# Optimization experiments

Hardware: AMD Instinct MI355X
Metric: run time of the kernel (lower is better)

Reference implementation:

```python
import jax, jax.numpy as jnp
import numpy as np

BS = 512
N_BOXES = 30   # num_boxes*3 in the torch module
K = 15
HID = 128
EMB = 64
FEAT = HID + EMB + 2  # 194


def _knn_idx(x, k):
    # x: (bs, n, 4); per-sample kNN (self excluded), matching pyg knn_graph with batch
    d = jnp.sum((x[:, :, None, :] - x[:, None, :, :]) ** 2, axis=-1)  # (bs, n, n)
    n = x.shape[1]
    d = d + jnp.eye(n, dtype=x.dtype) * 1e9  # exclude self-loops
    _, idx = jax.lax.top_k(-d, k)  # k nearest sources j for each target i
    return idx  # (bs, n, k)


def _edge_conv(x, idx, Wa, ba, Wb, bb):
    # EdgeConv: out_i = max_j mlp([x_i, x_j - x_i]), aggr='max'
    xj = jax.vmap(lambda xb, ib: xb[ib])(x, idx)            # (bs, n, k, F)
    xi = jnp.broadcast_to(x[:, :, None, :], xj.shape)        # (bs, n, k, F)
    m = jnp.concatenate([xi, xj - xi], axis=-1)              # (bs, n, k, 2F)
    h = jax.nn.relu(jnp.einsum('bnkf,hf->bnkh', m, Wa) + ba)
    h = jnp.einsum('bnkh,oh->bnko', h, Wb) + bb
    return jnp.max(h, axis=2)                                # (bs, n, HID)


def _q(nodes, emb, Wi, bi, Wma, bma, Wmb, bmb, Wca, bca, Wcb, bcb):
    bs, n, _ = nodes.shape
    idx = _knn_idx(nodes, K)
    cats = jnp.repeat(jnp.arange(3), n // 3)                 # [0]*10+[1]*10+[2]*10
    cls = jax.nn.relu(emb[cats])                             # (n, EMB)
    cls = jnp.broadcast_to(cls[None], (bs, n, EMB))
    tar = jnp.zeros((bs, n, 2), nodes.dtype)                 # tanh(zeros) = 0
    init = jnp.concatenate([jax.nn.relu(nodes @ Wi.T + bi), cls, tar], axis=-1)
    h = jax.nn.relu(_edge_conv(init, idx, Wma, bma, Wmb, bmb))
    h = jax.nn.relu(h @ Wca.T + bca)
    out = h @ Wcb.T + bcb                                    # (bs, n, 1)
    return out.reshape(bs, -1)


def setup_inputs() -> dict:
    key = jax.random.key(0)
    ks = jax.random.split(key, 22)
    rn = lambda k, shp: (jax.random.normal(k, shp) * 0.05).astype(jnp.float32)
    return {
        'state': jax.random.normal(ks[0], (BS, N_BOXES * 2), jnp.float32),
        'action': jax.random.normal(ks[1], (BS, N_BOXES * 2), jnp.float32),
        'W_init1': rn(ks[2], (HID, 4)), 'b_init1': rn(ks[3], (HID,)),
        'emb1': rn(ks[4], (3, EMB)),
        'W_m1a': rn(ks[5], (HID, 2 * FEAT)), 'b_m1a': rn(ks[6], (HID,)),
        'W_m1b': rn(ks[7], (HID, HID)), 'b_m1b': rn(ks[8], (HID,)),
        'W_c1a': rn(ks[9], (HID, HID)), 'b_c1a': rn(ks[10], (HID,)),
        'W_c1b': rn(ks[11], (1, HID)), 'b_c1b': rn(ks[12], (1,)),
        'W_init2': rn(ks[13], (HID, 4)), 'b_init2': rn(ks[14], (HID,)),
        'emb2': rn(ks[15], (3, EMB)),
        'W_c2a': rn(ks[16], (HID, HID)), 'b_c2a': rn(ks[17], (HID,)),
        'W_c2b': rn(ks[18], (1, HID)), 'b_c2b': rn(ks[19], (1,)),
    }


def reference(state, action, W_init1, b_init1, emb1, W_m1a, b_m1a, W_m1b, b_m1b,
              W_c1a, b_c1a, W_c1b, b_c1b, W_init2, b_init2, emb2,
              W_c2a, b_c2a, W_c2b, b_c2b):
    bs = state.shape[0]
    # Q1 node layout: interleaved per-box [sx, sy, ax, ay]
    nodes1 = jnp.concatenate([state.reshape(bs, N_BOXES, 2),
                              action.reshape(bs, N_BOXES, 2)], axis=-1)
    q1 = _q(nodes1, emb1, W_init1, b_init1, W_m1a, b_m1a, W_m1b, b_m1b,
            W_c1a, b_c1a, W_c1b, b_c1b)
    # Q2 node layout (faithful to torch bug): cat along dim 1 then view(-1, 4)
    nodes2 = jnp.concatenate([state, action], axis=1).reshape(bs, N_BOXES, 4)
    # conv1_2 reuses mlp1_1 weights (faithful to torch source)
    q2 = _q(nodes2, emb2, W_init2, b_init2, W_m1a, b_m1a, W_m1b, b_m1b,
            W_c2a, b_c2a, W_c2b, b_c2b)
    return (q1, q2)
```

## Files before the change

### kernel.cpp

```cpp
#include <hip/hip_runtime.h>

#define BSZ 512
#define NNODE 30
#define KNBR 15
#define HID 128
#define MTOT (BSZ*NNODE)

typedef __attribute__((ext_vector_type(8))) __bf16 bf16x8;
typedef __attribute__((ext_vector_type(4))) float f32x4;

__device__ __forceinline__ float frelu(float x){ return x > 0.f ? x : 0.f; }

__device__ __forceinline__ void node_coords(const float* __restrict__ st,
                                            const float* __restrict__ ac,
                                            int b, int n, int qsel, float c[4]) {
    if (qsel == 0) {
        c[0] = st[b*60 + 2*n];     c[1] = st[b*60 + 2*n + 1];
        c[2] = ac[b*60 + 2*n];     c[3] = ac[b*60 + 2*n + 1];
    } else {
        int base = 4*n;
        if (base < 60) {
            c[0]=st[b*60+base]; c[1]=st[b*60+base+1]; c[2]=st[b*60+base+2]; c[3]=st[b*60+base+3];
        } else {
            int a = base - 60;
            c[0]=ac[b*60+a]; c[1]=ac[b*60+a+1]; c[2]=ac[b*60+a+2]; c[3]=ac[b*60+a+3];
        }
    }
}

__global__ void k_prep(const float* __restrict__ Wa,  const float* __restrict__ Wb,
                       const float* __restrict__ Wca1,const float* __restrict__ Wca2,
                       const float* __restrict__ ba,
                       const float* __restrict__ emb1,const float* __restrict__ emb2,
                       __bf16* __restrict__ Wc16, __bf16* __restrict__ Wb16,
                       __bf16* __restrict__ Wca16_1, __bf16* __restrict__ Wca16_2,
                       float* __restrict__ cls1A, float* __restrict__ cls1B,
                       float* __restrict__ cls2A, float* __restrict__ cls2B) {
    int blk = blockIdx.x;
    if (blk < 320) {
        int t = blk*256 + threadIdx.x;
        if (t < 32768) {
            int o = t >> 7, h = t & 127;
            float v = (o < 128) ? (Wa[o*388 + h] - Wa[o*388 + 194 + h])
                                : Wa[(o-128)*388 + 194 + h];
            Wc16[t] = (__bf16)v;
        } else if (t < 49152) { int u = t - 32768; Wb16[u]    = (__bf16)Wb[u]; }
        else if (t < 65536)   { int u = t - 49152; Wca16_1[u] = (__bf16)Wca1[u]; }
        else                  { int u = t - 65536; Wca16_2[u] = (__bf16)Wca2[u]; }
    } else {
        int o = threadIdx.x;
        if (o >= 128) return;
        const float* emb = (blk == 320) ? emb1  : emb2;
        float* cA        = (blk == 320) ? cls1A : cls2A;
        float* cB        = (blk == 320) ? cls1B : cls2B;
        for (int c = 0; c < 3; ++c) {
            float sA = ba[o], sB = 0.f;
            for (int e = 0; e < 64; ++e) {
                float r  = frelu(emb[c*64 + e]);
                float wl = Wa[o*388 + 128 + e];
                float wr = Wa[o*388 + 194 + 128 + e];
                sA += (wl - wr) * r;
                sB += wr * r;
            }
            cA[c*128 + o] = sA;
            cB[c*128 + o] = sB;
        }
    }
}

__global__ void __launch_bounds__(256, 4) k_fused(
        const float* __restrict__ st, const float* __restrict__ ac,
        const float* __restrict__ Wi1, const float* __restrict__ bi1,
        const float* __restrict__ Wi2, const float* __restrict__ bi2,
        const __bf16* __restrict__ Wc16,
        const float* __restrict__ cls1A, const float* __restrict__ cls1B,
        const float* __restrict__ cls2A, const float* __restrict__ cls2B,
        const __bf16* __restrict__ Wb16, const float* __restrict__ bb,
        const __bf16* __restrict__ Wca16_1, const float* __restrict__ bca1,
        const float* __restrict__ Wcb1, const float* __restrict__ bcb1,
        const __bf16* __restrict__ Wca16_2, const float* __restrict__ bca2,
        const float* __restrict__ Wcb2, const float* __restrict__ bcb2,
        float* __restrict__ out) {
    __shared__ __align__(16) union UVE {
        __bf16 Vf[2][4][4][16][8];
        __bf16 El[32*136];
    } uVE;
    __shared__ __align__(16) __bf16 Al[30*136];
    __shared__ __align__(16) __bf16 Bl[30*136];
    __shared__ int idxs[30*16];
    __shared__ __align__(16) union UCR {
        float coords[30][4];
        float redh[4][16];
    } uCR;

    int tid  = threadIdx.x;
    int lane = tid & 63, wid = tid >> 6;
    int l15  = lane & 15, g = (lane >> 4) & 3;
    int bid  = blockIdx.x;
    int q    = bid >> 9, b = bid & 511;

    const float* Wi   = q ? Wi2 : Wi1;
    const float* bi   = q ? bi2 : bi1;
    const float* clsA = q ? cls2A : cls1A;
    const float* clsB = q ? cls2B : cls1B;
    const __bf16* Wca16 = q ? Wca16_2 : Wca16_1;
    const float* bca  = q ? bca2 : bca1;
    const float* Wcb  = q ? Wcb2 : Wcb1;
    const float* bcb  = q ? bcb2 : bcb1;

    if (tid < 30) {
        float c[4]; node_coords(st, ac, b, tid, q, c);
        uCR.coords[tid][0]=c[0]; uCR.coords[tid][1]=c[1];
        uCR.coords[tid][2]=c[2]; uCR.coords[tid][3]=c[3];
    }
    __syncthreads();

    if (tid < 30) {
        int i = tid;
        float ci0=uCR.coords[i][0], ci1=uCR.coords[i][1], ci2=uCR.coords[i][2], ci3=uCR.coords[i][3];
        float d[30];
        #pragma unroll
        for (int j = 0; j < 30; ++j) {
            float d0 = ci0-uCR.coords[j][0], d1 = ci1-uCR.coords[j][1];
            float d2 = ci2-uCR.coords[j][2], d3 = ci3-uCR.coords[j][3];
            d[j] = d0*d0 + d1*d1 + d2*d2 + d3*d3;
        }
        unsigned mask = 1u << i;
        for (int k = 0; k < KNBR; ++k) {
            float best = 3.4e38f; int bj = 0;
            #pragma unroll
            for (int j = 0; j < 30; ++j) {
                bool ok = !((mask >> j) & 1u) && (d[j] < best);
                if (ok) { best = d[j]; bj = j; }
            }
            mask |= 1u << bj;
            idxs[i*16 + k] = bj;
        }
        idxs[i*16 + 15] = idxs[i*16];
    } else if (tid >= 32) {
        for (int it = tid - 32; it < 512; it += 224) {
            int row = it & 15, g2 = (it >> 4) & 3, kk2 = (it >> 6) & 3, mt2 = it >> 8;
            int m = mt2*16 + row;
            bf16x8 v8;
            if (m < 30) {
                float c0=uCR.coords[m][0], c1=uCR.coords[m][1],
                      c2=uCR.coords[m][2], c3=uCR.coords[m][3];
                #pragma unroll
                for (int e = 0; e < 8; ++e) {
                    int h = kk2*32 + g2*8 + e;
                    v8[e] = (__bf16)frelu(bi[h] + Wi[h*4+0]*c0 + Wi[h*4+1]*c1
                                                + Wi[h*4+2]*c2 + Wi[h*4+3]*c3);
                }
            } else {
                #pragma unroll
                for (int e = 0; e < 8; ++e) v8[e] = (__bf16)0.f;
            }
            *(bf16x8*)&uVE.Vf[mt2][kk2][g2][row][0] = v8;
        }
    }
    __syncthreads();

    {
        int mt = wid & 1, half = wid >> 1;
        bf16x8 af[4];
        #pragma unroll
        for (int kk = 0; kk < 4; ++kk) af[kk] = *(const bf16x8*)&uVE.Vf[mt][kk][g][l15][0];
        f32x4 acc[8];
        #pragma unroll
        for (int nc = 0; nc < 8; ++nc) acc[nc] = (f32x4){0.f,0.f,0.f,0.f};
        #pragma unroll
        for (int nc = 0; nc < 8; ++nc) {
            int o256 = half*128 + nc*16 + l15;
            bf16x8 wf[4];
            #pragma unroll
            for (int kk = 0; kk < 4; ++kk)
                wf[kk] = *(const bf16x8*)(Wc16 + o256*128 + kk*32 + g*8);
            #pragma unroll
            for (int kk = 0; kk < 4; ++kk)
                acc[nc] = __builtin_amdgcn_mfma_f32_16x16x32_bf16(af[kk], wf[kk], acc[nc], 0, 0, 0);
        }
        const float* cls = half ? clsB : clsA;
        __bf16* dst = half ? Bl : Al;
        #pragma unroll
        for (int nc = 0; nc < 8; ++nc) {
            #pragma unroll
            for (int r = 0; r < 4; ++r) {
                int m = mt*16 + g*4 + r;
                if (m < 30) {
                    int o = nc*16 + l15;
                    int cat = m / 10;
                    dst[m*136 + o] = (__bf16)(acc[nc][r] + cls[cat*128 + o]);
                }
            }
        }
    }
    __syncthreads();

    {
        for (int ch = 0; ch < 2; ++ch) {
            bf16x8 wbf[4][4];
            #pragma unroll
            for (int oc = 0; oc < 4; ++oc)
                #pragma unroll
                for (int kk = 0; kk < 4; ++kk)
                    wbf[oc][kk] = *(const bf16x8*)(Wb16 + ((ch*4+oc)*16 + l15)*128 + kk*32 + g*8);
            float bbv[4];
            #pragma unroll
            for (int oc = 0; oc < 4; ++oc) bbv[oc] = bb[(ch*4+oc)*16 + l15];

            for (int i = wid; i < 30; i += 4) {
                int nb = idxs[i*16 + l15];
                bf16x8 hf[4];
                #pragma unroll
                for (int kk = 0; kk < 4; ++kk) {
                    bf16x8 pa = *(const bf16x8*)&Al[i*136  + kk*32 + g*8];
                    bf16x8 pb = *(const bf16x8*)&Bl[nb*136 + kk*32 + g*8];
                    bf16x8 h;
                    #pragma unroll
                    for (int e = 0; e < 8; ++e)
                        h[e] = (__bf16)frelu((float)pa[e] + (float)pb[e]);
                    hf[kk] = h;
                }
                f32x4 acc[4];
                #pragma unroll
                for (int oc = 0; oc < 4; ++oc) acc[oc] = (f32x4){0.f,0.f,0.f,0.f};
                #pragma unroll
                for (int kk = 0; kk < 4; ++kk)
                    #pragma unroll
                    for (int oc = 0; oc < 4; ++oc)
                        acc[oc] = __builtin_amdgcn_mfma_f32_16x16x32_bf16(hf[kk], wbf[oc][kk], acc[oc], 0, 0, 0);
                #pragma unroll
                for (int oc = 0; oc < 4; ++oc) {
                    float v = fmaxf(fmaxf(acc[oc][0], acc[oc][1]), fmaxf(acc[oc][2], acc[oc][3]));
                    v = fmaxf(v, __shfl_xor(v, 16));
                    v = fmaxf(v, __shfl_xor(v, 32));
                    if (g == 0) uVE.El[i*136 + (ch*4+oc)*16 + l15] = (__bf16)frelu(v + bbv[oc]);
                }
            }
        }
        if (tid < 136) ((unsigned*)uVE.El)[2040 + tid] = 0u;
    }
    __syncthreads();

    {
        int mt = wid & 1, half = wid >> 1;
        bf16x8 ef[4];
        #pragma unroll
        for (int kk = 0; kk < 4; ++kk)
            ef[kk] = *(const bf16x8*)&uVE.El[(mt*16 + l15)*136 + kk*32 + g*8];
        float s[4] = {0.f, 0.f, 0.f, 0.f};
        #pragma unroll
        for (int nc = 0; nc < 4; ++nc) {
            int o = half*64 + nc*16 + l15;
            bf16x8 wf[4];
            #pragma unroll
            for (int kk = 0; kk < 4; ++kk)
                wf[kk] = *(const bf16x8*)(Wca16 + o*128 + kk*32 + g*8);
            f32x4 a = (f32x4){0.f,0.f,0.f,0.f};
            #pragma unroll
            for (int kk = 0; kk < 4; ++kk)
                a = __builtin_amdgcn_mfma_f32_16x16x32_bf16(ef[kk], wf[kk], a, 0, 0, 0);
            float bcav = bca[o], wcbv = Wcb[o];
            #pragma unroll
            for (int r = 0; r < 4; ++r) s[r] += frelu(a[r] + bcav) * wcbv;
        }
        #pragma unroll
        for (int r = 0; r < 4; ++r) {
            s[r] += __shfl_xor(s[r], 1);
            s[r] += __shfl_xor(s[r], 2);
            s[r] += __shfl_xor(s[r], 4);
            s[r] += __shfl_xor(s[r], 8);
        }
        if (l15 == 0) {
            #pragma unroll
            for (int r = 0; r < 4; ++r) uCR.redh[wid][g*4 + r] = s[r];
        }
    }
    __syncthreads();
    if (tid < 30) {
        int mt = tid >> 4, mr = tid & 15;
        out[q*MTOT + b*30 + tid] = uCR.redh[mt][mr] + uCR.redh[mt+2][mr] + bcb[0];
    }
}

extern "C" void kernel_launch(void* const* d_in, const int* in_sizes, int n_in,
                              void* d_out, int out_size, void* d_ws, size_t ws_size,
                              hipStream_t stream) {
    const float* state  = (const float*)d_in[0];
    const float* action = (const float*)d_in[1];
    const float* W_init1= (const float*)d_in[2];
    const float* b_init1= (const float*)d_in[3];
    const float* emb1   = (const float*)d_in[4];
    const float* W_m1a  = (const float*)d_in[5];
    const float* b_m1a  = (const float*)d_in[6];
    const float* W_m1b  = (const float*)d_in[7];
    const float* b_m1b  = (const float*)d_in[8];
    const float* W_c1a  = (const float*)d_in[9];
    const float* b_c1a  = (const float*)d_in[10];
    const float* W_c1b  = (const float*)d_in[11];
    const float* b_c1b  = (const float*)d_in[12];
    const float* W_init2= (const float*)d_in[13];
    const float* b_init2= (const float*)d_in[14];
    const float* emb2   = (const float*)d_in[15];
    const float* W_c2a  = (const float*)d_in[16];
    const float* b_c2a  = (const float*)d_in[17];
    const float* W_c2b  = (const float*)d_in[18];
    const float* b_c2b  = (const float*)d_in[19];

    __bf16* Wc16    = (__bf16*)d_ws;
    __bf16* Wb16    = Wc16 + 32768;
    __bf16* Wca16_1 = Wb16 + 16384;
    __bf16* Wca16_2 = Wca16_1 + 16384;
    float*  cls1A   = (float*)(Wca16_2 + 16384);
    float*  cls1B   = cls1A + 384;
    float*  cls2A   = cls1B + 384;
    float*  cls2B   = cls2A + 384;
    float*  out     = (float*)d_out;

    k_prep<<<322, 256, 0, stream>>>(W_m1a, W_m1b, W_c1a, W_c2a, b_m1a, emb1, emb2,
                                    Wc16, Wb16, Wca16_1, Wca16_2,
                                    cls1A, cls1B, cls2A, cls2B);

    k_fused<<<2*BSZ, 256, 0, stream>>>(state, action,
                                       W_init1, b_init1, W_init2, b_init2,
                                       Wc16, cls1A, cls1B, cls2A, cls2B,
                                       Wb16, b_m1b,
                                       Wca16_1, b_c1a, W_c1b, b_c1b,
                                       Wca16_2, b_c2a, W_c2b, b_c2b,
                                       out);
}
```

Before: 172.7 us.

## Parallelize kNN via rank counting and split EdgeConv work across warps by output half

Replaces the serial per-thread kNN selection sort (30 threads doing 15 passes) with a block-wide pairwise distance table in shared memory and a rank-counting pass, so all 256 threads take part. The distance table shares a union with the Al buffer. The EdgeConv stage is also restructured so each warp owns half of the output channels and loads that half's weights once, instead of looping over two chunks and reloading weights. Tie-breaking by index keeps the neighbour ordering deterministic. The Al and Bl buffers grow to 32 rows, and the padding rows are now written unconditionally.

```diff
diff --git a/kernel.cpp b/kernel.cpp
--- a/kernel.cpp
+++ b/kernel.cpp
@@ -85,8 +85,11 @@
         __bf16 Vf[2][4][4][16][8];
         __bf16 El[32*136];
     } uVE;
-    __shared__ __align__(16) __bf16 Al[30*136];
-    __shared__ __align__(16) __bf16 Bl[30*136];
+    __shared__ __align__(16) union UDA {
+        float  dist[30*33];
+        __bf16 Al[32*136];
+    } uDA;
+    __shared__ __align__(16) __bf16 Bl[32*136];
     __shared__ int idxs[30*16];
     __shared__ __align__(16) union UCR {
         float coords[30][4];
@@ -115,51 +118,52 @@
     }
     __syncthreads();
 
-    if (tid < 30) {
-        int i = tid;
-        float ci0=uCR.coords[i][0], ci1=uCR.coords[i][1], ci2=uCR.coords[i][2], ci3=uCR.coords[i][3];
-        float d[30];
-        #pragma unroll
-        for (int j = 0; j < 30; ++j) {
-            float d0 = ci0-uCR.coords[j][0], d1 = ci1-uCR.coords[j][1];
-            float d2 = ci2-uCR.coords[j][2], d3 = ci3-uCR.coords[j][3];
-            d[j] = d0*d0 + d1*d1 + d2*d2 + d3*d3;
-        }
-        unsigned mask = 1u << i;
-        for (int k = 0; k < KNBR; ++k) {
-            float best = 3.4e38f; int bj = 0;
-            #pragma unroll
-            for (int j = 0; j < 30; ++j) {
-                bool ok = !((mask >> j) & 1u) && (d[j] < best);
-                if (ok) { best = d[j]; bj = j; }
-            }
-            mask |= 1u << bj;
-            idxs[i*16 + k] = bj;
-        }
-        idxs[i*16 + 15] = idxs[i*16];
-    } else if (tid >= 32) {
-        for (int it = tid - 32; it < 512; it += 224) {
-            int row = it & 15, g2 = (it >> 4) & 3, kk2 = (it >> 6) & 3, mt2 = it >> 8;
-            int m = mt2*16 + row;
-            bf16x8 v8;
-            if (m < 30) {
-                float c0=uCR.coords[m][0], c1=uCR.coords[m][1],
-                      c2=uCR.coords[m][2], c3=uCR.coords[m][3];
-                #pragma unroll
-                for (int e = 0; e < 8; ++e) {
-                    int h = kk2*32 + g2*8 + e;
-                    v8[e] = (__bf16)frelu(bi[h] + Wi[h*4+0]*c0 + Wi[h*4+1]*c1
-                                                + Wi[h*4+2]*c2 + Wi[h*4+3]*c3);
-                }
-            } else {
-                #pragma unroll
-                for (int e = 0; e < 8; ++e) v8[e] = (__bf16)0.f;
-            }
-            *(bf16x8*)&uVE.Vf[mt2][kk2][g2][row][0] = v8;
-        }
-    }
-    __syncthreads();
-
+    for (int t = tid; t < 900; t += 256) {
+        int i = t / 30, j = t - i*30;
+        float d0 = uCR.coords[i][0]-uCR.coords[j][0];
+        float d1 = uCR.coords[i][1]-uCR.coords[j][1];
+        float d2 = uCR.coords[i][2]-uCR.coords[j][2];
+        float d3 = uCR.coords[i][3]-uCR.coords[j][3];
+        uDA.dist[i*33 + j] = d0*d0 + d1*d1 + d2*d2 + d3*d3;
+    }
+    for (int it = tid; it < 512; it += 256) {
+        int row = it & 15, g2 = (it >> 4) & 3, kk2 = (it >> 6) & 3, mt2 = it >> 8;
+        int m = mt2*16 + row;
+        bf16x8 v8;
+        if (m < 30) {
+            float c0=uCR.coords[m][0], c1=uCR.coords[m][1],
+                  c2=uCR.coords[m][2], c3=uCR.coords[m][3];
+            #pragma unroll
+            for (int e = 0; e < 8; ++e) {
+                int h = kk2*32 + g2*8 + e;
+                v8[e] = (__bf16)frelu(bi[h] + Wi[h*4+0]*c0 + Wi[h*4+1]*c1
+                                            + Wi[h*4+2]*c2 + Wi[h*4+3]*c3);
+            }
+        } else {
+            #pragma unroll
+            for (int e = 0; e < 8; ++e) v8[e] = (__bf16)0.f;
+        }
+        *(bf16x8*)&uVE.Vf[mt2][kk2][g2][row][0] = v8;
+    }
+    __syncthreads();
+
+    for (int t = tid; t < 900; t += 256) {
+        int i = t / 30, j = t - i*30;
+        if (j != i) {
+            float dj = uDA.dist[i*33 + j];
+            int rank = 0;
+            #pragma unroll
+            for (int j2 = 0; j2 < 30; ++j2) {
+                float dv = uDA.dist[i*33 + j2];
+                bool less = (dv < dj) || (dv == dj && j2 < j);
+                rank += (j2 != i && less) ? 1 : 0;
+            }
+            if (rank < KNBR) idxs[i*16 + rank] = j;
+        }
+    }
+    __syncthreads();
+
+    if (tid < 30) idxs[tid*16 + 15] = idxs[tid*16];
     {
         int mt = wid & 1, half = wid >> 1;
         bf16x8 af[4];
@@ -180,62 +184,59 @@
                 acc[nc] = __builtin_amdgcn_mfma_f32_16x16x32_bf16(af[kk], wf[kk], acc[nc], 0, 0, 0);
         }
         const float* cls = half ? clsB : clsA;
-        __bf16* dst = half ? Bl : Al;
+        __bf16* dst = half ? Bl : uDA.Al;
         #pragma unroll
         for (int nc = 0; nc < 8; ++nc) {
             #pragma unroll
             for (int r = 0; r < 4; ++r) {
                 int m = mt*16 + g*4 + r;
-                if (m < 30) {
-                    int o = nc*16 + l15;
-                    int cat = m / 10;
-                    dst[m*136 + o] = (__bf16)(acc[nc][r] + cls[cat*128 + o]);
-                }
+                int o = nc*16 + l15;
+                int cat = (m < 30) ? (m / 10) : 0;
+                dst[m*136 + o] = (__bf16)(acc[nc][r] + cls[cat*128 + o]);
             }
         }
     }
     __syncthreads();
 
     {
-        for (int ch = 0; ch < 2; ++ch) {
-            bf16x8 wbf[4][4];
-            #pragma unroll
-            for (int oc = 0; oc < 4; ++oc)
+        int ip = wid & 1, oh = wid >> 1;
+        bf16x8 wbf[4][4];
+        #pragma unroll
+        for (int c = 0; c < 4; ++c)
+            #pragma unroll
+            for (int kk = 0; kk < 4; ++kk)
+                wbf[c][kk] = *(const bf16x8*)(Wb16 + ((oh*4+c)*16 + l15)*128 + kk*32 + g*8);
+        float bbv[4];
+        #pragma unroll
+        for (int c = 0; c < 4; ++c) bbv[c] = bb[(oh*4+c)*16 + l15];
+
+        for (int i = ip; i < 30; i += 2) {
+            int nb = idxs[i*16 + l15];
+            bf16x8 hf[4];
+            #pragma unroll
+            for (int kk = 0; kk < 4; ++kk) {
+                bf16x8 pa = *(const bf16x8*)&uDA.Al[i*136  + kk*32 + g*8];
+                bf16x8 pb = *(const bf16x8*)&Bl[nb*136 + kk*32 + g*8];
+                bf16x8 h;
                 #pragma unroll
-                for (int kk = 0; kk < 4; ++kk)
-                    wbf[oc][kk] = *(const bf16x8*)(Wb16 + ((ch*4+oc)*16 + l15)*128 + kk*32 + g*8);
-            float bbv[4];
-            #pragma unroll
-            for (int oc = 0; oc < 4; ++oc) bbv[oc] = bb[(ch*4+oc)*16 + l15];
-
-            for (int i = wid; i < 30; i += 4) {
-                int nb = idxs[i*16 + l15];
-                bf16x8 hf[4];
+                for (int e = 0; e < 8; ++e)
+                    h[e] = (__bf16)frelu((float)pa[e] + (float)pb[e]);
+                hf[kk] = h;
+            }
+            f32x4 acc[4];
+            #pragma unroll
+            for (int c = 0; c < 4; ++c) acc[c] = (f32x4){0.f,0.f,0.f,0.f};
+            #pragma unroll
+            for (int kk = 0; kk < 4; ++kk)
                 #pragma unroll
-                for (int kk = 0; kk < 4; ++kk) {
-                    bf16x8 pa = *(const bf16x8*)&Al[i*136  + kk*32 + g*8];
-                    bf16x8 pb = *(const bf16x8*)&Bl[nb*136 + kk*32 + g*8];
-                    bf16x8 h;
-                    #pragma unroll
-                    for (int e = 0; e < 8; ++e)
-                        h[e] = (__bf16)frelu((float)pa[e] + (float)pb[e]);
-                    hf[kk] = h;
-                }
-                f32x4 acc[4];
-                #pragma unroll
-                for (int oc = 0; oc < 4; ++oc) acc[oc] = (f32x4){0.f,0.f,0.f,0.f};
-                #pragma unroll
-                for (int kk = 0; kk < 4; ++kk)
-                    #pragma unroll
-                    for (int oc = 0; oc < 4; ++oc)
-                        acc[oc] = __builtin_amdgcn_mfma_f32_16x16x32_bf16(hf[kk], wbf[oc][kk], acc[oc], 0, 0, 0);
-                #pragma unroll
-                for (int oc = 0; oc < 4; ++oc) {
-                    float v = fmaxf(fmaxf(acc[oc][0], acc[oc][1]), fmaxf(acc[oc][2], acc[oc][3]));
-                    v = fmaxf(v, __shfl_xor(v, 16));
-                    v = fmaxf(v, __shfl_xor(v, 32));
-                    if (g == 0) uVE.El[i*136 + (ch*4+oc)*16 + l15] = (__bf16)frelu(v + bbv[oc]);
-                }
+                for (int c = 0; c < 4; ++c)
+                    acc[c] = __builtin_amdgcn_mfma_f32_16x16x32_bf16(hf[kk], wbf[c][kk], acc[c], 0, 0, 0);
+            #pragma unroll
+            for (int c = 0; c < 4; ++c) {
+                float v = fmaxf(fmaxf(acc[c][0], acc[c][1]), fmaxf(acc[c][2], acc[c][3]));
+                v = fmaxf(v, __shfl_xor(v, 16));
+                v = fmaxf(v, __shfl_xor(v, 32));
+                if (g == 0) uVE.El[i*136 + (oh*4+c)*16 + l15] = (__bf16)frelu(v + bbv[c]);
             }
         }
         if (tid < 136) ((unsigned*)uVE.El)[2040 + tid] = 0u;
```

Result: no change. 172.0 us (-0.4%).
